# Optimization experiments

Measured on AMD Instinct MI355X. Metric: run time of the kernel, lower is better.

## Reference

```python
import jax, jax.numpy as jnp
import numpy as np


def get_rel_pos(q_size, k_size, rel_pos):
    # sizes are static python ints; rel_pos has length 2*max(q_size,k_size)-1
    q_ratio = max(k_size / q_size, 1.0)
    k_ratio = max(q_size / k_size, 1.0)
    dist = (np.arange(q_size)[:, None] * q_ratio
            - (np.arange(k_size)[None, :] + (1.0 - k_size)) * k_ratio).astype(np.int64)
    return rel_pos[dist]  # [q_size, k_size, head_dim]


def decomposed_rel_pos_3d(qh, q_thw, k_thw, rel_pos_t, rel_pos_h, rel_pos_w):
    # qh: [B, Q, n_heads, head_dim]
    q_t, q_h, q_w = q_thw
    k_t, k_h, k_w = k_thw
    Rt = get_rel_pos(q_t, k_t, rel_pos_t)
    Rh = get_rel_pos(q_h, k_h, rel_pos_h)
    Rw = get_rel_pos(q_w, k_w, rel_pos_w)
    B = qh.shape[0]
    n, c = qh.shape[2], qh.shape[3]
    q6 = qh.reshape(B, q_t, q_h, q_w, n, c)
    rel_t = jnp.einsum('bthwnc,tkc->bnthwk', q6, Rt)
    rel_h = jnp.einsum('bthwnc,hkc->bnthwk', q6, Rh)
    rel_w = jnp.einsum('bthwnc,wkc->bnthwk', q6, Rw)
    bias = (rel_t[:, :, :, :, :, :, None, None]
            + rel_h[:, :, :, :, :, None, :, None]
            + rel_w[:, :, :, :, :, None, None, :])
    return bias.reshape(B, n, q_t * q_h * q_w, k_t * k_h * k_w)


def setup_inputs() -> dict:
    key = jax.random.key(0)
    ks = jax.random.split(key, 16)
    B, dim, num_heads = 2, 768, 12
    head_dim = dim // num_heads
    q_thw = (8, 14, 14)
    k_thw = (8, 14, 14)
    Q = q_thw[0] * q_thw[1] * q_thw[2]
    K = k_thw[0] * k_thw[1] * k_thw[2]
    s = 0.02
    inp = {
        'q': jax.random.normal(ks[0], (B, Q, dim), jnp.float32),
        'k': jax.random.normal(ks[1], (B, K, dim), jnp.float32),
        'Wq': jax.random.normal(ks[2], (dim, dim), jnp.float32) * s,
        'bq': jnp.zeros((dim,), jnp.float32),
        'Wk': jax.random.normal(ks[3], (dim, dim), jnp.float32) * s,
        'bk': jnp.zeros((dim,), jnp.float32),
        'Wv': jax.random.normal(ks[4], (dim, dim), jnp.float32) * s,
        'bv': jnp.zeros((dim,), jnp.float32),
        'Wo': jax.random.normal(ks[5], (dim, dim), jnp.float32) * s,
        'bo': jnp.zeros((dim,), jnp.float32),
        'rel_pos_t': jax.random.normal(ks[6], (2 * max(q_thw[0], k_thw[0]) - 1, head_dim), jnp.float32) * s,
        'rel_pos_h': jax.random.normal(ks[7], (2 * max(q_thw[1], k_thw[1]) - 1, head_dim), jnp.float32) * s,
        'rel_pos_w': jax.random.normal(ks[8], (2 * max(q_thw[2], k_thw[2]) - 1, head_dim), jnp.float32) * s,
        'q_t': q_thw[0], 'q_h': q_thw[1], 'q_w': q_thw[2],
        'k_t': k_thw[0], 'k_h': k_thw[1], 'k_w': k_thw[2],
    }
    return inp


def reference(q, k, Wq, bq, Wk, bk, Wv, bv, Wo, bo,
              rel_pos_t, rel_pos_h, rel_pos_w,
              q_t, q_h, q_w, k_t, k_h, k_w):
    B, Q, dim = q.shape
    num_heads = 12
    c = dim // num_heads
    scale = 1.0 / np.sqrt(c).astype(np.float32)
    qh = (q @ Wq.T + bq).reshape(B, -1, num_heads, c)   # [B,Q,n,c]
    vh = (k @ Wv.T + bv).reshape(B, -1, num_heads, c)   # [B,K,n,c]
    kh = (k @ Wk.T + bk).reshape(B, -1, num_heads, c)   # [B,K,n,c]
    bias = decomposed_rel_pos_3d(qh, (q_t, q_h, q_w), (k_t, k_h, k_w),
                                 rel_pos_t, rel_pos_h, rel_pos_w)  # [B,n,Q,K]
    scores = jnp.einsum('bqnc,bknc->bnqk', qh, kh) * scale + bias
    attn = jax.nn.softmax(scores, axis=-1)
    out = jnp.einsum('bnqk,bknc->bqnc', attn, vh).reshape(B, Q, dim)
    return out @ Wo.T + bo
```

## Files before the change

kernel.cpp:

```cpp
#include <hip/hip_runtime.h>
#include <math.h>

typedef __bf16 bf16_t;
typedef __bf16 bf16x4 __attribute__((ext_vector_type(4)));
typedef __bf16 bf16x8 __attribute__((ext_vector_type(8)));
typedef float floatx4 __attribute__((ext_vector_type(4)));

#define MFMA16(A, B, C) __builtin_amdgcn_mfma_f32_16x16x32_bf16((A), (B), (C), 0, 0, 0)

static constexpr int BB  = 2;
static constexpr int NH  = 12;
static constexpr int HD  = 64;
static constexpr int DIM = 768;
static constexpr int QS  = 1568;
static constexpr int KS  = 1568;
static constexpr int KSP = 1664;
static constexpr int MROWS = BB * QS;
static constexpr int KT  = 32;
static constexpr int TD  = 80;

static constexpr float LOG2E = 1.4426950408889634f;
static constexpr float SCALE_L2E = 0.125f * LOG2E;

__device__ __forceinline__ void async16(const void* g, void* l) {
    __builtin_amdgcn_global_load_lds(
        (const __attribute__((address_space(1))) unsigned int*)g,
        (__attribute__((address_space(3))) unsigned int*)l, 16, 0, 0);
}

__global__ __launch_bounds__(256) void cvt_w(
    const float* __restrict__ q, const float* __restrict__ k,
    const float* __restrict__ wq, const float* __restrict__ wk,
    const float* __restrict__ wv, const float* __restrict__ wo,
    const float* __restrict__ rpt, const float* __restrict__ rph,
    const float* __restrict__ rpw,
    bf16_t* __restrict__ Wb, bf16_t* __restrict__ qb, bf16_t* __restrict__ kb,
    bf16_t* __restrict__ koh, bf16_t* __restrict__ Tt, bf16_t* __restrict__ vT)
{
    const int NW4 = DIM * DIM / 4;
    const int NX4 = MROWS * DIM / 4;
    const int PADC = (KSP - KS) / 8;
    int i = blockIdx.x * 256 + threadIdx.x;
    if (i < 4 * NW4) {
        const int w = i / NW4;
        const int off = i - w * NW4;
        const float* src = (w == 0) ? wq : (w == 1) ? wk : (w == 2) ? wv : wo;
        floatx4 v = ((const floatx4*)src)[off];
        bf16x4 o;
#pragma unroll
        for (int r = 0; r < 4; ++r) o[r] = (bf16_t)v[r];
        ((bf16x4*)(Wb + (size_t)w * DIM * DIM))[off] = o;
        return;
    }
    i -= 4 * NW4;
    if (i < 2 * NX4) {
        const float* src = (i < NX4) ? q : k;
        bf16_t* dst = (i < NX4) ? qb : kb;
        const int off = (i < NX4) ? i : i - NX4;
        floatx4 v = ((const floatx4*)src)[off];
        bf16x4 o;
#pragma unroll
        for (int r = 0; r < 4; ++r) o[r] = (bf16_t)v[r];
        ((bf16x4*)dst)[off] = o;
        return;
    }
    i -= 2 * NX4;
    if (i < KS) {
        const int key = i;
        const int tk = key / 196;
        const int rem = key - tk * 196;
        const int hk = rem / 14;
        const int wk_ = rem - hk * 14;
#pragma unroll
        for (int c8 = 0; c8 < 8; ++c8) {
            bf16x8 v;
#pragma unroll
            for (int j = 0; j < 8; ++j) {
                const int e = c8 * 8 + j;
                const float f = (e == tk || e == 8 + hk || e == 22 + wk_) ? 1.f : 0.f;
                v[j] = (bf16_t)f;
            }
            *(bf16x8*)(koh + (size_t)key * 64 + c8 * 8) = v;
        }
        return;
    }
    i -= KS;
    if (i < TD * 8) {
        const int d = i >> 3;
        const int c8 = (i & 7) * 8;
        bf16x8 v;
#pragma unroll
        for (int j = 0; j < 8; ++j) {
            const int c = c8 + j;
            float f = 0.f;
            if (d < 15)      f = LOG2E * rpt[(size_t)d * 64 + c];
            else if (d < 42) f = LOG2E * rph[(size_t)(d - 15) * 64 + c];
            else if (d < 69) f = LOG2E * rpw[(size_t)(d - 42) * 64 + c];
            v[j] = (bf16_t)f;
        }
        *(bf16x8*)(Tt + (size_t)d * 64 + c8) = v;
        return;
    }
    i -= TD * 8;
    if (i < BB * NH * HD * PADC) {
        const int row = i / PADC;
        const int ch  = i - row * PADC;
        bf16x8 z;
#pragma unroll
        for (int r = 0; r < 8; ++r) z[r] = (bf16_t)0.f;
        *(bf16x8*)(vT + (size_t)row * KSP + KS + ch * 8) = z;
    }
}

__global__ __launch_bounds__(256) void gemm_qkv(
    const bf16_t* __restrict__ qb, const bf16_t* __restrict__ kb,
    const bf16_t* __restrict__ Wb,
    const float* __restrict__ bq, const float* __restrict__ bk,
    const float* __restrict__ bv,
    bf16_t* __restrict__ qhP, bf16_t* __restrict__ khP, bf16_t* __restrict__ vT)
{
    __shared__ __align__(16) bf16_t Asa[128 * 64];
    __shared__ __align__(16) bf16_t Asb[128 * 64];
    __shared__ __align__(16) bf16_t Bsa[64 * 64];
    __shared__ __align__(16) bf16_t Bsb[64 * 64];

    const int tid   = threadIdx.x;
    const int lane  = tid & 63;
    const int wave  = tid >> 6;
    const int row16 = lane & 15;
    const int quad  = lane >> 4;
    const int wm    = wave & 1;
    const int wn    = wave >> 1;
    const int m0 = blockIdx.x * 128;
    const int yb = blockIdx.y;
    const int proj = yb / 12;
    const int n0 = (yb - proj * 12) * 64;

    const bf16_t* X = (proj == 0) ? qb : kb;
    const bf16_t* W = Wb + (size_t)proj * DIM * DIM;
    const float* bias = (proj == 0) ? bq : (proj == 1) ? bk : bv;
    const float osc = (proj == 1) ? SCALE_L2E : 1.0f;

    floatx4 acc[4][2];
#pragma unroll
    for (int mt = 0; mt < 4; ++mt)
#pragma unroll
        for (int nt = 0; nt < 2; ++nt) acc[mt][nt] = (floatx4){0.f, 0.f, 0.f, 0.f};

    auto stage = [&](int k0, bf16_t* An, bf16_t* Bn) {
#pragma unroll
        for (int p = 0; p < 4; ++p) {
            const int s = p * 256 + tid;
            const int row = s >> 3, c = s & 7;
            const int g = c ^ (row & 7);
            const int rowc = min(m0 + row, MROWS - 1);
            async16(X + (size_t)rowc * DIM + k0 + g * 8, An + s * 8);
        }
#pragma unroll
        for (int p = 0; p < 2; ++p) {
            const int s = p * 256 + tid;
            const int row = s >> 3, c = s & 7;
            const int g = c ^ (row & 7);
            async16(W + (size_t)(n0 + row) * DIM + k0 + g * 8, Bn + s * 8);
        }
    };

    auto body = [&](int k0, const bf16_t* Ac, const bf16_t* Bc,
                    bf16_t* An, bf16_t* Bn, bool pf) {
        __syncthreads();
        if (pf) stage(k0 + 64, An, Bn);
#pragma unroll
        for (int h = 0; h < 2; ++h) {
            const int pa = (h * 4 + quad) ^ (row16 & 7);
            bf16x8 aF[4], bF[2];
#pragma unroll
            for (int mt = 0; mt < 4; ++mt) {
                const int rowA = wm * 64 + mt * 16 + row16;
                aF[mt] = *(const bf16x8*)&Ac[rowA * 64 + pa * 8];
            }
#pragma unroll
            for (int nt = 0; nt < 2; ++nt) {
                const int rowB = wn * 32 + nt * 16 + row16;
                bF[nt] = *(const bf16x8*)&Bc[rowB * 64 + pa * 8];
            }
#pragma unroll
            for (int mt = 0; mt < 4; ++mt)
#pragma unroll
                for (int nt = 0; nt < 2; ++nt)
                    acc[mt][nt] = MFMA16(aF[mt], bF[nt], acc[mt][nt]);
        }
    };

    stage(0, Asa, Bsa);
    for (int ii = 0; ii < 6; ++ii) {
        const int k0 = ii * 128;
        body(k0,      Asa, Bsa, Asb, Bsb, true);
        body(k0 + 64, Asb, Bsb, Asa, Bsa, k0 + 128 < DIM);
    }

#pragma unroll
    for (int nt = 0; nt < 2; ++nt) {
        const int col = n0 + wn * 32 + nt * 16 + row16;
        const int head = col >> 6, cl = col & 63;
        const float bv_ = bias[col];
#pragma unroll
        for (int mt = 0; mt < 4; ++mt) {
            const int row0 = m0 + wm * 64 + mt * 16 + quad * 4;
            if (row0 < MROWS) {
                const int bb = (row0 >= KS) ? 1 : 0;
                const int key0 = row0 - bb * KS;
                if (proj == 2) {
                    bf16x4 pv;
#pragma unroll
                    for (int r = 0; r < 4; ++r) pv[r] = (bf16_t)(acc[mt][nt][r] + bv_);
                    *(bf16x4*)&vT[((size_t)(bb * NH + head) * 64 + cl) * KSP + key0] = pv;
                } else {
                    bf16_t* dst = (proj == 0) ? qhP : khP;
#pragma unroll
                    for (int r = 0; r < 4; ++r)
                        dst[((size_t)(bb * NH + head) * KS + key0 + r) * 64 + cl] =
                            (bf16_t)((acc[mt][nt][r] + bv_) * osc);
                }
            }
        }
    }
}

__global__ __launch_bounds__(256) void qext(
    const bf16_t* __restrict__ qhP, const bf16_t* __restrict__ Tt,
    bf16_t* __restrict__ Qe)
{
    __shared__ float Gs[64][81];

    const int tid   = threadIdx.x;
    const int lane  = tid & 63;
    const int wave  = tid >> 6;
    const int row16 = lane & 15;
    const int quad  = lane >> 4;
    const int m0 = blockIdx.x * 64;

    const bf16_t* ap = qhP + (size_t)(m0 + wave * 16 + row16) * 64 + quad * 8;
    bf16x8 a0 = *(const bf16x8*)(ap);
    bf16x8 a1 = *(const bf16x8*)(ap + 32);

    floatx4 acc[5];
#pragma unroll
    for (int t = 0; t < 5; ++t) {
        const bf16_t* tp = Tt + (size_t)(t * 16 + row16) * 64 + quad * 8;
        floatx4 s = (floatx4){0.f, 0.f, 0.f, 0.f};
        s = MFMA16(a0, *(const bf16x8*)(tp), s);
        s = MFMA16(a1, *(const bf16x8*)(tp + 32), s);
        acc[t] = s;
    }
#pragma unroll
    for (int t = 0; t < 5; ++t)
#pragma unroll
        for (int r = 0; r < 4; ++r)
            Gs[wave * 16 + quad * 4 + r][t * 16 + row16] = acc[t][r];
    __syncthreads();

#pragma unroll
    for (int ii = 0; ii < 16; ++ii) {
        const int i = ii * 256 + tid;
        const int row = i >> 6, e = i & 63;
        const int grow = m0 + row;
        const int qg = grow % QS;
        const int tq = qg / 196;
        const int rem = qg - tq * 196;
        const int hq = rem / 14;
        const int wq = rem - hq * 14;
        int d;
        if (e < 8)       d = tq - e + 7;
        else if (e < 22) d = 15 + hq - (e - 8) + 13;
        else             d = 42 + wq - (e - 22) + 13;
        const float val = (e < 36) ? Gs[row][d] : 0.f;
        Qe[(size_t)grow * 64 + e] = (bf16_t)val;
    }
}

__global__ __launch_bounds__(128, 3) void attn_fused(
    const bf16_t* __restrict__ qhP, const bf16_t* __restrict__ Qe,
    const bf16_t* __restrict__ khP, const bf16_t* __restrict__ koh,
    const bf16_t* __restrict__ vT, bf16_t* __restrict__ ao)
{
    __shared__ __align__(16) bf16_t KsA[32 * 128];
    __shared__ __align__(16) bf16_t KsB[32 * 128];
    __shared__ __align__(16) bf16_t VsA[64 * 32];
    __shared__ __align__(16) bf16_t VsB[64 * 32];
    __shared__ __align__(16) bf16_t Pl[2 * 16 * 40];

    const int tid   = threadIdx.x;
    const int lane  = tid & 63;
    const int wave  = tid >> 6;
    const int row16 = lane & 15;
    const int quad  = lane >> 4;

    const int L = blockIdx.x;
    const int xcd = L & 7;
    const int j = L >> 3;
    const int bn = xcd * 3 + (j % 3);
    const int q0 = (j / 3) * 32;
    const int b = bn / NH;
    const int n = bn - b * NH;

    const int qrow = q0 + wave * 16 + row16;
    const bf16_t* qp = qhP + ((size_t)bn * QS + qrow) * 64 + quad * 8;
    const bf16_t* qe = Qe  + ((size_t)bn * QS + qrow) * 64 + quad * 8;
    bf16x8 aQ0 = *(const bf16x8*)(qp);
    bf16x8 aQ1 = *(const bf16x8*)(qp + 32);
    bf16x8 aQ2 = *(const bf16x8*)(qe);
    bf16x8 aQ3 = *(const bf16x8*)(qe + 32);

    floatx4 O[4];
#pragma unroll
    for (int ct = 0; ct < 4; ++ct) O[ct] = (floatx4){0.f, 0.f, 0.f, 0.f};
    float lsum[4] = {0.f, 0.f, 0.f, 0.f};

    const bf16_t* khb = khP + (size_t)bn * KS * 64;
    const bf16_t* vTb = vT + (size_t)bn * 64 * KSP;
    const int pbase = wave * 16 * 40;
    const int sw3 = row16 & 7;
    const int sw2 = (row16 >> 1) & 3;

    auto stageKV = [&](int k0, bf16_t* Kn, bf16_t* Vn) {
#pragma unroll
        for (int p = 0; p < 4; ++p) {
            const int s = p * 128 + tid;
            const int row = s >> 4, c = s & 15;
            const int l = c ^ (row & 7);
            const bf16_t* src = (l < 8)
                ? khb + (size_t)(k0 + row) * 64 + l * 8
                : koh + (size_t)(k0 + row) * 64 + (l - 8) * 8;
            async16(src, Kn + s * 8);
        }
#pragma unroll
        for (int p = 0; p < 2; ++p) {
            const int s = p * 128 + tid;
            const int row = s >> 2, c = s & 3;
            const int l = c ^ ((row >> 1) & 3);
            async16(vTb + (size_t)row * KSP + k0 + l * 8, Vn + s * 8);
        }
    };

    auto iter = [&](int ki, const bf16_t* Kc, const bf16_t* Vc,
                    bf16_t* Kn, bf16_t* Vn, bool pf) {
        const int k0 = ki * KT;
        __syncthreads();
        if (pf) stageKV(k0 + KT, Kn, Vn);

        floatx4 S[2];
#pragma unroll
        for (int t = 0; t < 2; ++t) {
            const bf16_t* kp_ = &Kc[(t * 16 + row16) * 128];
            floatx4 sA = (floatx4){0.f, 0.f, 0.f, 0.f};
            floatx4 sB = (floatx4){0.f, 0.f, 0.f, 0.f};
            sA = MFMA16(aQ0, *(const bf16x8*)&kp_[((0 + quad) ^ sw3) * 8], sA);
            sB = MFMA16(aQ2, *(const bf16x8*)&kp_[((8 + quad) ^ sw3) * 8], sB);
            sA = MFMA16(aQ1, *(const bf16x8*)&kp_[((4 + quad) ^ sw3) * 8], sA);
            sB = MFMA16(aQ3, *(const bf16x8*)&kp_[((12 + quad) ^ sw3) * 8], sB);
            S[t] = sA + sB;
        }

#pragma unroll
        for (int t = 0; t < 2; ++t) {
#pragma unroll
            for (int r = 0; r < 4; ++r) {
                float p = __builtin_amdgcn_exp2f(S[t][r]);
                lsum[r] += p;
                Pl[pbase + (quad * 4 + r) * 40 + t * 16 + row16] = (bf16_t)p;
            }
        }

        bf16x8 aP = *(const bf16x8*)&Pl[pbase + row16 * 40 + quad * 8];
#pragma unroll
        for (int ct = 0; ct < 4; ++ct) {
            bf16x8 bV = *(const bf16x8*)&Vc[(ct * 16 + row16) * 32 + (quad ^ sw2) * 8];
            O[ct] = MFMA16(aP, bV, O[ct]);
        }
    };

    stageKV(0, KsA, VsA);
#pragma unroll 1
    for (int kp2 = 0; kp2 < 24; ++kp2) {
        iter(2 * kp2,     KsA, VsA, KsB, VsB, true);
        iter(2 * kp2 + 1, KsB, VsB, KsA, VsA, true);
    }
    iter(48, KsA, VsA, KsB, VsB, false);

    float inv[4];
#pragma unroll
    for (int r = 0; r < 4; ++r) {
        float l = lsum[r];
        l += __shfl_xor(l, 1);
        l += __shfl_xor(l, 2);
        l += __shfl_xor(l, 4);
        l += __shfl_xor(l, 8);
        inv[r] = 1.f / l;
    }
#pragma unroll
    for (int ct = 0; ct < 4; ++ct) {
        const int c = n * HD + ct * 16 + row16;
#pragma unroll
        for (int r = 0; r < 4; ++r) {
            const int qr = q0 + wave * 16 + quad * 4 + r;
            ao[(size_t)(b * QS + qr) * DIM + c] = (bf16_t)(O[ct][r] * inv[r]);
        }
    }
}

__global__ __launch_bounds__(256) void gemm_o(
    const bf16_t* __restrict__ X, const bf16_t* __restrict__ W,
    const float* __restrict__ bias, float* __restrict__ Y)
{
    __shared__ __align__(16) bf16_t Asa[64 * 64];
    __shared__ __align__(16) bf16_t Asb[64 * 64];
    __shared__ __align__(16) bf16_t Bsa[64 * 64];
    __shared__ __align__(16) bf16_t Bsb[64 * 64];

    const int tid   = threadIdx.x;
    const int lane  = tid & 63;
    const int wave  = tid >> 6;
    const int row16 = lane & 15;
    const int quad  = lane >> 4;
    const int m0 = blockIdx.x * 64;
    const int n0 = blockIdx.y * 64;

    floatx4 acc[4];
#pragma unroll
    for (int nt = 0; nt < 4; ++nt) acc[nt] = (floatx4){0.f, 0.f, 0.f, 0.f};

    auto stage = [&](int k0, bf16_t* An, bf16_t* Bn) {
#pragma unroll
        for (int p = 0; p < 2; ++p) {
            const int s = p * 256 + tid;
            const int row = s >> 3, pc = s & 7;
            const int g = pc ^ (row & 7);
            async16(X + (size_t)(m0 + row) * DIM + k0 + g * 8, An + s * 8);
            async16(W + (size_t)(n0 + row) * DIM + k0 + g * 8, Bn + s * 8);
        }
    };

    auto body = [&](int k0, const bf16_t* Ac, const bf16_t* Bc,
                    bf16_t* An, bf16_t* Bn, bool pf) {
        __syncthreads();
        if (pf) stage(k0 + 64, An, Bn);
#pragma unroll
        for (int h = 0; h < 2; ++h) {
            const int lc = h * 4 + quad;
            const int pa = lc ^ (row16 & 7);
            const int rowA = wave * 16 + row16;
            bf16x8 aF = *(const bf16x8*)&Ac[rowA * 64 + pa * 8];
#pragma unroll
            for (int nt = 0; nt < 4; ++nt) {
                bf16x8 bF = *(const bf16x8*)&Bc[(nt * 16 + row16) * 64 + pa * 8];
                acc[nt] = MFMA16(aF, bF, acc[nt]);
            }
        }
    };

    stage(0, Asa, Bsa);
    for (int ii = 0; ii < 6; ++ii) {
        const int k0 = ii * 128;
        body(k0,      Asa, Bsa, Asb, Bsb, true);
        body(k0 + 64, Asb, Bsb, Asa, Bsa, k0 + 128 < DIM);
    }

#pragma unroll
    for (int nt = 0; nt < 4; ++nt) {
        const int col = n0 + nt * 16 + row16;
        const float bv = bias[col];
#pragma unroll
        for (int r = 0; r < 4; ++r) {
            const int row = m0 + wave * 16 + quad * 4 + r;
            Y[(size_t)row * DIM + col] = acc[nt][r] + bv;
        }
    }
}

extern "C" void kernel_launch(void* const* d_in, const int* in_sizes, int n_in,
                              void* d_out, int out_size, void* d_ws, size_t ws_size,
                              hipStream_t stream) {
    const float* q   = (const float*)d_in[0];
    const float* k   = (const float*)d_in[1];
    const float* Wq  = (const float*)d_in[2];
    const float* bq  = (const float*)d_in[3];
    const float* Wk  = (const float*)d_in[4];
    const float* bk  = (const float*)d_in[5];
    const float* Wv  = (const float*)d_in[6];
    const float* bv  = (const float*)d_in[7];
    const float* Wo  = (const float*)d_in[8];
    const float* bo  = (const float*)d_in[9];
    const float* rpt = (const float*)d_in[10];
    const float* rph = (const float*)d_in[11];
    const float* rpw = (const float*)d_in[12];

    bf16_t* qhP  = (bf16_t*)d_ws;
    bf16_t* khP  = qhP  + (size_t)MROWS * DIM;
    bf16_t* vT   = khP  + (size_t)MROWS * DIM;
    bf16_t* QeKb = vT   + (size_t)BB * NH * HD * KSP;
    bf16_t* aoQb = QeKb + (size_t)MROWS * DIM;
    bf16_t* koh  = aoQb + (size_t)MROWS * DIM;
    bf16_t* Tt   = koh  + (size_t)KS * 64;
    bf16_t* Wb   = Tt   + (size_t)TD * 64;

    const int NW4 = DIM * DIM / 4;
    const int NX4 = MROWS * DIM / 4;
    const int PADC = (KSP - KS) / 8;
    const int NCVT = 4 * NW4 + 2 * NX4 + KS + TD * 8 + BB * NH * HD * PADC;
    cvt_w<<<(NCVT + 255) / 256, 256, 0, stream>>>(
        q, k, Wq, Wk, Wv, Wo, rpt, rph, rpw, Wb, aoQb, QeKb, koh, Tt, vT);

    gemm_qkv<<<dim3(25, 36), 256, 0, stream>>>(
        aoQb, QeKb, Wb, bq, bk, bv, qhP, khP, vT);

    qext<<<(BB * NH * QS) / 64, 256, 0, stream>>>(qhP, Tt, QeKb);

    attn_fused<<<dim3(8 * 3 * 49), 128, 0, stream>>>(
        qhP, QeKb, khP, koh, vT, aoQb);

    gemm_o<<<dim3(MROWS / 64, DIM / 64), 256, 0, stream>>>(
        aoQb, Wb + (size_t)3 * DIM * DIM, bo, (float*)d_out);
}
```

Baseline: 213.9 us.

## Enlarge attention and output-projection tiles, load V directly from global memory

The attention kernel now uses 4 waves per block covering 64 query rows, so each staged K tile is shared by twice as many rows, with clamping and guards for the ragged last tile. V is no longer staged through shared memory; each wave reads its V fragments straight from global memory into registers every iteration. The output projection GEMM moves to 128x64 tiles with a 2x2 wave layout, which raises register reuse, and adds row clamping and guarding for the partial last tile. Risks are uncoalesced or redundant global V reads across waves, extra wasted work in the padded last query tile, and fewer blocks to spread across the GPU.

```diff
diff --git a/kernel.cpp b/kernel.cpp
--- a/kernel.cpp
+++ b/kernel.cpp
@@ -278,16 +278,14 @@
     }
 }
 
-__global__ __launch_bounds__(128, 3) void attn_fused(
+__global__ __launch_bounds__(256, 2) void attn_fused(
     const bf16_t* __restrict__ qhP, const bf16_t* __restrict__ Qe,
     const bf16_t* __restrict__ khP, const bf16_t* __restrict__ koh,
     const bf16_t* __restrict__ vT, bf16_t* __restrict__ ao)
 {
     __shared__ __align__(16) bf16_t KsA[32 * 128];
     __shared__ __align__(16) bf16_t KsB[32 * 128];
-    __shared__ __align__(16) bf16_t VsA[64 * 32];
-    __shared__ __align__(16) bf16_t VsB[64 * 32];
-    __shared__ __align__(16) bf16_t Pl[2 * 16 * 40];
+    __shared__ __align__(16) bf16_t Pl[4 * 16 * 40];
 
     const int tid   = threadIdx.x;
     const int lane  = tid & 63;
@@ -299,11 +297,11 @@
     const int xcd = L & 7;
     const int j = L >> 3;
     const int bn = xcd * 3 + (j % 3);
-    const int q0 = (j / 3) * 32;
+    const int q0 = (j / 3) * 64;
     const int b = bn / NH;
     const int n = bn - b * NH;
 
-    const int qrow = q0 + wave * 16 + row16;
+    const int qrow = min(q0 + wave * 16 + row16, QS - 1);
     const bf16_t* qp = qhP + ((size_t)bn * QS + qrow) * 64 + quad * 8;
     const bf16_t* qe = Qe  + ((size_t)bn * QS + qrow) * 64 + quad * 8;
     bf16x8 aQ0 = *(const bf16x8*)(qp);
@@ -320,12 +318,11 @@
     const bf16_t* vTb = vT + (size_t)bn * 64 * KSP;
     const int pbase = wave * 16 * 40;
     const int sw3 = row16 & 7;
-    const int sw2 = (row16 >> 1) & 3;
-
-    auto stageKV = [&](int k0, bf16_t* Kn, bf16_t* Vn) {
-#pragma unroll
-        for (int p = 0; p < 4; ++p) {
-            const int s = p * 128 + tid;
+
+    auto stageK = [&](int k0, bf16_t* Kn) {
+#pragma unroll
+        for (int p = 0; p < 2; ++p) {
+            const int s = p * 256 + tid;
             const int row = s >> 4, c = s & 15;
             const int l = c ^ (row & 7);
             const bf16_t* src = (l < 8)
@@ -333,20 +330,18 @@
                 : koh + (size_t)(k0 + row) * 64 + (l - 8) * 8;
             async16(src, Kn + s * 8);
         }
-#pragma unroll
-        for (int p = 0; p < 2; ++p) {
-            const int s = p * 128 + tid;
-            const int row = s >> 2, c = s & 3;
-            const int l = c ^ ((row >> 1) & 3);
-            async16(vTb + (size_t)row * KSP + k0 + l * 8, Vn + s * 8);
-        }
     };
 
-    auto iter = [&](int ki, const bf16_t* Kc, const bf16_t* Vc,
-                    bf16_t* Kn, bf16_t* Vn, bool pf) {
+    auto iter = [&](int ki, const bf16_t* Kc, bf16_t* Kn, bool pf) {
         const int k0 = ki * KT;
         __syncthreads();
-        if (pf) stageKV(k0 + KT, Kn, Vn);
+        if (pf) stageK(k0 + KT, Kn);
+
+        bf16x8 vf[4];
+#pragma unroll
+        for (int ct = 0; ct < 4; ++ct)
+            vf[ct] = *(const bf16x8*)(vTb + (size_t)(ct * 16 + row16) * KSP
+                                      + k0 + quad * 8);
 
         floatx4 S[2];
 #pragma unroll
@@ -373,19 +368,17 @@
 
         bf16x8 aP = *(const bf16x8*)&Pl[pbase + row16 * 40 + quad * 8];
 #pragma unroll
-        for (int ct = 0; ct < 4; ++ct) {
-            bf16x8 bV = *(const bf16x8*)&Vc[(ct * 16 + row16) * 32 + (quad ^ sw2) * 8];
-            O[ct] = MFMA16(aP, bV, O[ct]);
-        }
+        for (int ct = 0; ct < 4; ++ct)
+            O[ct] = MFMA16(aP, vf[ct], O[ct]);
     };
 
-    stageKV(0, KsA, VsA);
+    stageK(0, KsA);
 #pragma unroll 1
     for (int kp2 = 0; kp2 < 24; ++kp2) {
-        iter(2 * kp2,     KsA, VsA, KsB, VsB, true);
-        iter(2 * kp2 + 1, KsB, VsB, KsA, VsA, true);
-    }
-    iter(48, KsA, VsA, KsB, VsB, false);
+        iter(2 * kp2,     KsA, KsB, true);
+        iter(2 * kp2 + 1, KsB, KsA, true);
+    }
+    iter(48, KsA, KsB, false);
 
     float inv[4];
 #pragma unroll
@@ -403,7 +396,8 @@
 #pragma unroll
         for (int r = 0; r < 4; ++r) {
             const int qr = q0 + wave * 16 + quad * 4 + r;
-            ao[(size_t)(b * QS + qr) * DIM + c] = (bf16_t)(O[ct][r] * inv[r]);
+            if (qr < QS)
+                ao[(size_t)(b * QS + qr) * DIM + c] = (bf16_t)(O[ct][r] * inv[r]);
         }
     }
 }
@@ -412,8 +406,8 @@
     const bf16_t* __restrict__ X, const bf16_t* __restrict__ W,
     const float* __restrict__ bias, float* __restrict__ Y)
 {
-    __shared__ __align__(16) bf16_t Asa[64 * 64];
-    __shared__ __align__(16) bf16_t Asb[64 * 64];
+    __shared__ __align__(16) bf16_t Asa[128 * 64];
+    __shared__ __align__(16) bf16_t Asb[128 * 64];
     __shared__ __align__(16) bf16_t Bsa[64 * 64];
     __shared__ __align__(16) bf16_t Bsb[64 * 64];
 
@@ -422,20 +416,31 @@
     const int wave  = tid >> 6;
     const int row16 = lane & 15;
     const int quad  = lane >> 4;
-    const int m0 = blockIdx.x * 64;
+    const int wm    = wave & 1;
+    const int wn    = wave >> 1;
+    const int m0 = blockIdx.x * 128;
     const int n0 = blockIdx.y * 64;
 
-    floatx4 acc[4];
-#pragma unroll
-    for (int nt = 0; nt < 4; ++nt) acc[nt] = (floatx4){0.f, 0.f, 0.f, 0.f};
+    floatx4 acc[4][2];
+#pragma unroll
+    for (int mt = 0; mt < 4; ++mt)
+#pragma unroll
+        for (int nt = 0; nt < 2; ++nt) acc[mt][nt] = (floatx4){0.f, 0.f, 0.f, 0.f};
 
     auto stage = [&](int k0, bf16_t* An, bf16_t* Bn) {
+#pragma unroll
+        for (int p = 0; p < 4; ++p) {
+            const int s = p * 256 + tid;
+            const int row = s >> 3, c = s & 7;
+            const int g = c ^ (row & 7);
+            const int rowc = min(m0 + row, MROWS - 1);
+            async16(X + (size_t)rowc * DIM + k0 + g * 8, An + s * 8);
+        }
 #pragma unroll
         for (int p = 0; p < 2; ++p) {
             const int s = p * 256 + tid;
-            const int row = s >> 3, pc = s & 7;
-            const int g = pc ^ (row & 7);
-            async16(X + (size_t)(m0 + row) * DIM + k0 + g * 8, An + s * 8);
+            const int row = s >> 3, c = s & 7;
+            const int g = c ^ (row & 7);
             async16(W + (size_t)(n0 + row) * DIM + k0 + g * 8, Bn + s * 8);
         }
     };
@@ -446,15 +451,23 @@
         if (pf) stage(k0 + 64, An, Bn);
 #pragma unroll
         for (int h = 0; h < 2; ++h) {
-            const int lc = h * 4 + quad;
-            const int pa = lc ^ (row16 & 7);
-            const int rowA = wave * 16 + row16;
-            bf16x8 aF = *(const bf16x8*)&Ac[rowA * 64 + pa * 8];
-#pragma unroll
-            for (int nt = 0; nt < 4; ++nt) {
-                bf16x8 bF = *(const bf16x8*)&Bc[(nt * 16 + row16) * 64 + pa * 8];
-                acc[nt] = MFMA16(aF, bF, acc[nt]);
-            }
+            const int pa = (h * 4 + quad) ^ (row16 & 7);
+            bf16x8 aF[4], bF[2];
+#pragma unroll
+            for (int mt = 0; mt < 4; ++mt) {
+                const int rowA = wm * 64 + mt * 16 + row16;
+                aF[mt] = *(const bf16x8*)&Ac[rowA * 64 + pa * 8];
+            }
+#pragma unroll
+            for (int nt = 0; nt < 2; ++nt) {
+                const int rowB = wn * 32 + nt * 16 + row16;
+                bF[nt] = *(const bf16x8*)&Bc[rowB * 64 + pa * 8];
+            }
+#pragma unroll
+            for (int mt = 0; mt < 4; ++mt)
+#pragma unroll
+                for (int nt = 0; nt < 2; ++nt)
+                    acc[mt][nt] = MFMA16(aF[mt], bF[nt], acc[mt][nt]);
         }
     };
 
@@ -466,13 +479,17 @@
     }
 
 #pragma unroll
-    for (int nt = 0; nt < 4; ++nt) {
-        const int col = n0 + nt * 16 + row16;
+    for (int nt = 0; nt < 2; ++nt) {
+        const int col = n0 + wn * 32 + nt * 16 + row16;
         const float bv = bias[col];
 #pragma unroll
-        for (int r = 0; r < 4; ++r) {
-            const int row = m0 + wave * 16 + quad * 4 + r;
-            Y[(size_t)row * DIM + col] = acc[nt][r] + bv;
+        for (int mt = 0; mt < 4; ++mt) {
+            const int row0 = m0 + wm * 64 + mt * 16 + quad * 4;
+            if (row0 < MROWS) {
+#pragma unroll
+                for (int r = 0; r < 4; ++r)
+                    Y[(size_t)(row0 + r) * DIM + col] = acc[mt][nt][r] + bv;
+            }
         }
     }
 }
@@ -515,9 +532,9 @@
 
     qext<<<(BB * NH * QS) / 64, 256, 0, stream>>>(qhP, Tt, QeKb);
 
-    attn_fused<<<dim3(8 * 3 * 49), 128, 0, stream>>>(
+    attn_fused<<<dim3(8 * 3 * 25), 256, 0, stream>>>(
         qhP, QeKb, khP, koh, vT, aoQb);
 
-    gemm_o<<<dim3(MROWS / 64, DIM / 64), 256, 0, stream>>>(
+    gemm_o<<<dim3(25, 12), 256, 0, stream>>>(
         aoQb, Wb + (size_t)3 * DIM * DIM, bo, (float*)d_out);
 }
```

After: 245.2 us. +14.6%, slower.
